# Kernel optimization log

Measured on AMD Instinct MI355X. Metric: run time of the kernel, lower is better.

The kernel has to match this reference:

```python
import jax, jax.numpy as jnp
import numpy as np

H = 16       # num heads
HD = 64      # head dim
D = H * HD   # hidden size

def _rotate_half(x):
    x1, x2 = jnp.split(x, 2, axis=-1)
    return jnp.concatenate([-x2, x1], axis=-1)

def setup_inputs() -> dict:
    key = jax.random.key(0)
    ks = jax.random.split(key, 12)
    B, N, NP = 16, 1029, 1024  # batch, tokens (5 prefix + 1024 patches), patch tokens
    inp = {
        "hidden_states": jax.random.normal(ks[0], (B, N, D), dtype=jnp.float32),
        "sin": jax.random.uniform(ks[1], (NP, HD), dtype=jnp.float32, minval=-1.0, maxval=1.0),
        "cos": jax.random.uniform(ks[2], (NP, HD), dtype=jnp.float32, minval=-1.0, maxval=1.0),
        "Wq": jax.random.normal(ks[3], (D, D), dtype=jnp.float32) * 0.02,
        "bq": jnp.zeros((D,), dtype=jnp.float32),
        "Wk": jax.random.normal(ks[4], (D, D), dtype=jnp.float32) * 0.02,
        "bk": jnp.zeros((D,), dtype=jnp.float32),
        "Wv": jax.random.normal(ks[5], (D, D), dtype=jnp.float32) * 0.02,
        "bv": jnp.zeros((D,), dtype=jnp.float32),
        "Wo": jax.random.normal(ks[6], (D, D), dtype=jnp.float32) * 0.02,
        "bo": jnp.zeros((D,), dtype=jnp.float32),
    }
    return inp

def reference(hidden_states, sin, cos, Wq, bq, Wk, bk, Wv, bv, Wo, bo):
    B, N, _ = hidden_states.shape
    scaling = HD ** -0.5
    # qkv projections (nn.Linear: x @ W.T + b), split to heads: [B,H,N,HD]
    def proj(W, b):
        y = hidden_states @ W.T + b
        return y.reshape(B, N, H, HD).transpose(0, 2, 1, 3)
    q, k, v = proj(Wq, bq), proj(Wk, bk), proj(Wv, bv)
    # rotary pos emb on patch-token suffix only
    prefix = N - sin.shape[-2]
    def rope(x):
        xs = x[:, :, prefix:, :]
        xs = xs * cos + _rotate_half(xs) * sin
        return jnp.concatenate([x[:, :, :prefix, :], xs], axis=2)
    q, k = rope(q), rope(k)
    # eager attention: softmax in fp32
    attn = jnp.einsum("bhqd,bhkd->bhqk", q, k) * scaling
    attn = jax.nn.softmax(attn.astype(jnp.float32), axis=-1).astype(q.dtype)
    out = jnp.einsum("bhqk,bhkd->bhqd", attn, v)
    out = out.transpose(0, 2, 1, 3).reshape(B, N, D)
    return out @ Wo.T + bo
```

## Files before the change

### kernel.cpp

```cpp
#include <hip/hip_runtime.h>
#include <stdint.h>

#define H 16
#define HD 64
#define D 1024
#define NTOK 1029
#define BATCH 16
#define NPAD 1152
#define M_ROWS (BATCH*NTOK)
#define MPAD 16512
#define KB 1024
#define PREFIX 5

typedef unsigned short u16;
typedef __attribute__((ext_vector_type(8))) short short8;
typedef __attribute__((ext_vector_type(4))) short short4v;
typedef __attribute__((ext_vector_type(4))) float float4v;
typedef __attribute__((ext_vector_type(4))) unsigned int uint4v;

__device__ __forceinline__ u16 f2bf(float x) {
  unsigned int u = __float_as_uint(x);
  u += 0x7FFFu + ((u >> 16) & 1u);
  return (u16)(u >> 16);
}

__device__ __forceinline__ void gload16(const void* g, void* l) {
  __builtin_amdgcn_global_load_lds((const __attribute__((address_space(1))) void*)g,
                                   (__attribute__((address_space(3))) void*)l, 16, 0, 0);
}

__global__ __launch_bounds__(256) void cvt_A_kernel(const float* __restrict__ src,
                                                    u16* __restrict__ dst) {
  int idx = blockIdx.x * 256 + threadIdx.x;
  int m = idx >> 8, k = (idx & 255) * 4;
  float4v x = (float4v)0.f;
  if (m < M_ROWS) x = *(const float4v*)(src + (size_t)m * D + k);
  short4v o;
#pragma unroll
  for (int j = 0; j < 4; j++) o[j] = (short)f2bf(x[j]);
  *(short4v*)(dst + (size_t)m * D + k) = o;
}

__global__ __launch_bounds__(256) void cvt_W_kernel(
    const float* __restrict__ w0, const float* __restrict__ w1,
    const float* __restrict__ w2, const float* __restrict__ w3,
    u16* __restrict__ e0, u16* __restrict__ e1, u16* __restrict__ e2, u16* __restrict__ e3) {
  const float* src = (blockIdx.y == 0) ? w0 : (blockIdx.y == 1) ? w1 : (blockIdx.y == 2) ? w2 : w3;
  u16* dst = (blockIdx.y == 0) ? e0 : (blockIdx.y == 1) ? e1 : (blockIdx.y == 2) ? e2 : e3;
  int idx = blockIdx.x * 256 + threadIdx.x;
  int m = idx >> 8, k = (idx & 255) * 4;
  float4v x = *(const float4v*)(src + (size_t)m * D + k);
  short4v o;
#pragma unroll
  for (int j = 0; j < 4; j++) o[j] = (short)f2bf(x[j]);
  *(short4v*)(dst + (size_t)m * D + k) = o;
}

__device__ __forceinline__ void gemm_mainloop(const u16* __restrict__ A,
                                              const u16* __restrict__ Bw,
                                              u16* As, u16* Bs, int mtile, int ntile,
                                              float4v acc[4][4]) {
  const int tid = threadIdx.x;
  const int lane = tid & 63;
  const int wave = tid >> 6;
  const int wm = (wave >> 1) * 64;
  const int wn = (wave & 1) * 64;
  const int ar = lane & 15;
  const int kq = lane >> 4;
#pragma unroll
  for (int i = 0; i < 4; i++)
#pragma unroll
    for (int j = 0; j < 4; j++) acc[i][j] = (float4v)0.f;

  const size_t abase = (size_t)mtile * 128 * KB;
  const size_t bbase = (size_t)ntile * 128 * KB;
  for (int k0 = 0; k0 < KB; k0 += 32) {
    __syncthreads();
#pragma unroll
    for (int i = 0; i < 2; i++) {
      int chunk = i * 256 + tid;
      gload16(A + abase + (size_t)(chunk >> 2) * KB + k0 + (chunk & 3) * 8,
              As + (size_t)(i * 256 + (tid & ~63)) * 8);
      gload16(Bw + bbase + (size_t)(chunk >> 2) * KB + k0 + (chunk & 3) * 8,
              Bs + (size_t)(i * 256 + (tid & ~63)) * 8);
    }
    __syncthreads();
    short8 af[4], bf[4];
#pragma unroll
    for (int ms = 0; ms < 4; ms++)
      af[ms] = *(const short8*)(As + (wm + ms * 16 + ar) * 32 + kq * 8);
#pragma unroll
    for (int ns = 0; ns < 4; ns++)
      bf[ns] = *(const short8*)(Bs + (wn + ns * 16 + ar) * 32 + kq * 8);
#pragma unroll
    for (int ms = 0; ms < 4; ms++)
#pragma unroll
      for (int ns = 0; ns < 4; ns++)
        acc[ms][ns] = __builtin_amdgcn_mfma_f32_16x16x32_bf16(af[ms], bf[ns], acc[ms][ns], 0, 0, 0);
  }
}

__global__ __launch_bounds__(256) void gemm_qkv_kernel(
    const u16* __restrict__ A,
    const u16* __restrict__ Wqb, const u16* __restrict__ Wkb, const u16* __restrict__ Wvb,
    const float* __restrict__ bq, const float* __restrict__ bk, const float* __restrict__ bv,
    const float* __restrict__ sinp, const float* __restrict__ cosp,
    u16* __restrict__ qb, u16* __restrict__ kb, u16* __restrict__ vt) {
  __shared__ __align__(16) u16 As[128 * 32];
  __shared__ __align__(16) u16 Bs[128 * 32];
  const int z = blockIdx.z;
  const u16* Bw = (z == 0) ? Wqb : (z == 1) ? Wkb : Wvb;
  const float* bias = (z == 0) ? bq : (z == 1) ? bk : bv;
  const int ntile = blockIdx.x, mtile = blockIdx.y;
  float4v acc[4][4];
  gemm_mainloop(A, Bw, As, Bs, mtile, ntile, acc);

  const int tid = threadIdx.x, lane = tid & 63, wave = tid >> 6;
  const int wm = (wave >> 1) * 64, wn = (wave & 1) * 64;
  const int ar = lane & 15, kq = lane >> 4;
#pragma unroll
  for (int ms = 0; ms < 4; ms++) {
#pragma unroll
    for (int r = 0; r < 4; r++) {
      int grow = mtile * 128 + wm + ms * 16 + kq * 4 + r;
      if (grow >= M_ROWS) continue;
      int b = grow / NTOK;
      int n = grow - b * NTOK;
      bool dorope = (z != 2) && (n >= PREFIX);
      int pos = n - PREFIX;
#pragma unroll
      for (int ns = 0; ns < 4; ns++) {
        int col = ntile * 128 + wn + ns * 16 + ar;
        int hh = col >> 6, d = col & 63;
        float y = acc[ms][ns][r] + bias[col];
        if (z == 2) {
          vt[((size_t)(b * H + hh) * 64 + d) * NPAD + n] = f2bf(y);
          continue;
        }
        if (dorope) {
          float xp = acc[ms][ns ^ 2][r] + bias[col ^ 32];
          float c = cosp[pos * HD + d], s = sinp[pos * HD + d];
          y = y * c + ((d < 32) ? -xp : xp) * s;
        }
        if (z == 0) y *= 0.125f;
        u16* outp = (z == 0) ? qb : kb;
        outp[((size_t)(b * H + hh) * NPAD + n) * 64 + d] = f2bf(y);
      }
    }
  }
}

#define SSHIFT 3.0f
#define NJT 17
__global__ __launch_bounds__(256) void attn_kernel(const u16* __restrict__ qb,
                                                   const u16* __restrict__ kb,
                                                   const u16* __restrict__ vt,
                                                   u16* __restrict__ ao) {
  __shared__ __align__(16) u16 sQ[128 * 72];
  __shared__ __align__(16) u16 sK[64 * 72];
  __shared__ __align__(16) u16 sV[64 * 72];
  const int tid = threadIdx.x, lane = tid & 63, wave = tid >> 6;
  const int ar = lane & 15, kq = lane >> 4;
  const int qt = blockIdx.x, hh = blockIdx.y, b = blockIdx.z;
  const int bh = b * H + hh;
  const u16* qbase = qb + (size_t)bh * NPAD * 64;
  const u16* kbase = kb + (size_t)bh * NPAD * 64;
  const u16* vbase = vt + (size_t)bh * 64 * NPAD;

#pragma unroll
  for (int i = 0; i < 4; i++) {
    int chunk = i * 256 + tid;
    int row = chunk >> 3, c = chunk & 7;
    *(uint4v*)(sQ + row * 72 + c * 8) =
        *(const uint4v*)(qbase + (size_t)(qt * 128 + row) * 64 + c * 8);
  }
  __syncthreads();
  short8 aq[2][2];
#pragma unroll
  for (int ms = 0; ms < 2; ms++)
#pragma unroll
    for (int ki = 0; ki < 2; ki++)
      aq[ms][ki] = *(const short8*)(sQ + (wave * 32 + ms * 16 + ar) * 72 + ki * 32 + kq * 8);
  u16* sP = sQ + wave * 32 * 72;

  float rs[2][4];
  float4v o_acc[2][4];
#pragma unroll
  for (int ms = 0; ms < 2; ms++)
#pragma unroll
    for (int r = 0; r < 4; r++) rs[ms][r] = 0.f;
#pragma unroll
  for (int ms = 0; ms < 2; ms++)
#pragma unroll
    for (int t = 0; t < 4; t++) o_acc[ms][t] = (float4v)0.f;

  for (int jt = 0; jt < NJT; jt++) {
    __syncthreads();
#pragma unroll
    for (int i = 0; i < 2; i++) {
      int chunk = i * 256 + tid;
      int row = chunk >> 3, c = chunk & 7;
      *(uint4v*)(sK + row * 72 + c * 8) =
          *(const uint4v*)(kbase + (size_t)(jt * 64 + row) * 64 + c * 8);
      *(uint4v*)(sV + row * 72 + c * 8) =
          *(const uint4v*)(vbase + (size_t)row * NPAD + jt * 64 + c * 8);
    }
    __syncthreads();

    float4v s[2][4];
#pragma unroll
    for (int ms = 0; ms < 2; ms++)
#pragma unroll
      for (int t = 0; t < 4; t++) s[ms][t] = (float4v)0.f;
#pragma unroll
    for (int ki = 0; ki < 2; ki++) {
#pragma unroll
      for (int t = 0; t < 4; t++) {
        short8 bk8 = *(const short8*)(sK + (t * 16 + ar) * 72 + ki * 32 + kq * 8);
#pragma unroll
        for (int ms = 0; ms < 2; ms++)
          s[ms][t] = __builtin_amdgcn_mfma_f32_16x16x32_bf16(aq[ms][ki], bk8, s[ms][t], 0, 0, 0);
      }
    }
    if (jt == NJT - 1) {
#pragma unroll
      for (int t = 0; t < 4; t++)
        if ((NJT - 1) * 64 + t * 16 + ar >= NTOK) {
#pragma unroll
          for (int ms = 0; ms < 2; ms++) s[ms][t] = (float4v)(-INFINITY);
        }
    }
    asm volatile("" ::: "memory");
#pragma unroll
    for (int ms = 0; ms < 2; ms++)
#pragma unroll
      for (int t = 0; t < 4; t++)
#pragma unroll
        for (int r = 0; r < 4; r++) {
          float p = __expf(s[ms][t][r] - SSHIFT);
          rs[ms][r] += p;
          sP[(ms * 16 + kq * 4 + r) * 72 + t * 16 + ar] = f2bf(p);
        }
    asm volatile("" ::: "memory");
#pragma unroll
    for (int ki = 0; ki < 2; ki++) {
#pragma unroll
      for (int ms = 0; ms < 2; ms++) {
        short8 ap = *(const short8*)(sP + (ms * 16 + ar) * 72 + ki * 32 + kq * 8);
#pragma unroll
        for (int t = 0; t < 4; t++) {
          short8 bv8 = *(const short8*)(sV + (t * 16 + ar) * 72 + ki * 32 + kq * 8);
          o_acc[ms][t] = __builtin_amdgcn_mfma_f32_16x16x32_bf16(ap, bv8, o_acc[ms][t], 0, 0, 0);
        }
      }
    }
  }
#pragma unroll
  for (int ms = 0; ms < 2; ms++)
#pragma unroll
    for (int r = 0; r < 4; r++) {
      float l = rs[ms][r];
#pragma unroll
      for (int off = 1; off < 16; off <<= 1) l += __shfl_xor(l, off, 64);
      int i = qt * 128 + wave * 32 + ms * 16 + kq * 4 + r;
      if (i >= NTOK) continue;
      float inv = 1.f / l;
      size_t mg = (size_t)b * NTOK + i;
#pragma unroll
      for (int t = 0; t < 4; t++)
        ao[mg * D + hh * 64 + t * 16 + ar] = f2bf(o_acc[ms][t][r] * inv);
    }
}

__global__ __launch_bounds__(256) void gemm_o_kernel(const u16* __restrict__ A,
                                                     const u16* __restrict__ Wob,
                                                     const float* __restrict__ bo,
                                                     float* __restrict__ out) {
  __shared__ __align__(16) u16 As[128 * 32];
  __shared__ __align__(16) u16 Bs[128 * 32];
  const int ntile = blockIdx.x, mtile = blockIdx.y;
  float4v acc[4][4];
  gemm_mainloop(A, Wob, As, Bs, mtile, ntile, acc);
  const int tid = threadIdx.x, lane = tid & 63, wave = tid >> 6;
  const int wm = (wave >> 1) * 64, wn = (wave & 1) * 64;
  const int ar = lane & 15, kq = lane >> 4;
#pragma unroll
  for (int ms = 0; ms < 4; ms++)
#pragma unroll
    for (int r = 0; r < 4; r++) {
      int grow = mtile * 128 + wm + ms * 16 + kq * 4 + r;
      if (grow >= M_ROWS) continue;
#pragma unroll
      for (int ns = 0; ns < 4; ns++) {
        int col = ntile * 128 + wn + ns * 16 + ar;
        out[(size_t)grow * D + col] = acc[ms][ns][r] + bo[col];
      }
    }
}

extern "C" void kernel_launch(void* const* d_in, const int* in_sizes, int n_in,
                              void* d_out, int out_size, void* d_ws, size_t ws_size,
                              hipStream_t stream) {
  const float* hidden = (const float*)d_in[0];
  const float* sinp = (const float*)d_in[1];
  const float* cosp = (const float*)d_in[2];
  const float* Wq = (const float*)d_in[3]; const float* bq = (const float*)d_in[4];
  const float* Wk = (const float*)d_in[5]; const float* bk = (const float*)d_in[6];
  const float* Wv = (const float*)d_in[7]; const float* bv = (const float*)d_in[8];
  const float* Wo = (const float*)d_in[9]; const float* bo = (const float*)d_in[10];
  float* out = (float*)d_out;
  (void)in_sizes; (void)n_in; (void)out_size; (void)ws_size;

  char* ws = (char*)d_ws;
  size_t off = 0;
  auto carve = [&](size_t elems) {
    u16* p = (u16*)(ws + off);
    off += ((elems * 2 + 255) & ~(size_t)255);
    return p;
  };
  u16* A_bf = carve((size_t)MPAD * KB);
  u16* Wqb = carve((size_t)D * KB);
  u16* Wkb = carve((size_t)D * KB);
  u16* Wvb = carve((size_t)D * KB);
  u16* Wob = carve((size_t)D * KB);
  u16* q_b = carve((size_t)BATCH * H * NPAD * 64);
  u16* k_b = carve((size_t)BATCH * H * NPAD * 64);
  u16* v_t = carve((size_t)BATCH * H * NPAD * 64);

  hipLaunchKernelGGL(cvt_A_kernel, dim3(MPAD), dim3(256), 0, stream, hidden, A_bf);
  hipLaunchKernelGGL(cvt_W_kernel, dim3(1024, 4), dim3(256), 0, stream,
                     Wq, Wk, Wv, Wo, Wqb, Wkb, Wvb, Wob);
  hipLaunchKernelGGL(gemm_qkv_kernel, dim3(8, 129, 3), dim3(256), 0, stream,
                     A_bf, Wqb, Wkb, Wvb, bq, bk, bv, sinp, cosp, q_b, k_b, v_t);
  hipLaunchKernelGGL(attn_kernel, dim3(9, H, BATCH), dim3(256), 0, stream, q_b, k_b, v_t, A_bf);
  hipLaunchKernelGGL(gemm_o_kernel, dim3(8, 129), dim3(256), 0, stream, A_bf, Wob, bo, out);
}
```

Before: 611.6 us.

## Rewrite projection GEMMs with 256x256 tiles, double-buffered LDS and swizzle

Replaces the 128x128, K=32 single-buffered GEMM mainloop with a 256x256 tile, K=64 stage, 8-wave kernel. Global-to-LDS loads are double-buffered and prefetched two stages ahead, and a XOR swizzle on the LDS layout avoids bank conflicts. Phased MFMA blocks use barriers and setprio to interleave the waves. This raises arithmetic intensity and overlaps loads with compute in both the QKV and output projections. It also uses much more LDS (128KB per block) and more registers, and pads MPAD so the 256-row tiles fit.

```diff
diff --git a/kernel.cpp b/kernel.cpp
--- a/kernel.cpp
+++ b/kernel.cpp
@@ -8,7 +8,8 @@
 #define BATCH 16
 #define NPAD 1152
 #define M_ROWS (BATCH*NTOK)
-#define MPAD 16512
+#define MPAD 16640
+#define MT256 65
 #define KB 1024
 #define PREFIX 5
 
@@ -56,73 +57,111 @@
   *(short4v*)(dst + (size_t)m * D + k) = o;
 }
 
-__device__ __forceinline__ void gemm_mainloop(const u16* __restrict__ A,
-                                              const u16* __restrict__ Bw,
-                                              u16* As, u16* Bs, int mtile, int ntile,
-                                              float4v acc[4][4]) {
+
+__device__ __forceinline__ void stage256(const u16* __restrict__ gA, const u16* __restrict__ gB,
+                                         u16* dA, u16* dB, int dwo) {
+#pragma unroll
+  for (int i = 0; i < 4; i++)
+    gload16(gA + (size_t)i * 64 * KB, dA + i * 4096 + dwo);
+#pragma unroll
+  for (int i = 0; i < 4; i++)
+    gload16(gB + (size_t)i * 64 * KB, dB + i * 4096 + dwo);
+}
+
+#define GPHASE(mh, soffv, loadB)                                                          \
+  {                                                                                       \
+    short8 afr[4];                                                                        \
+    _Pragma("unroll") for (int m4 = 0; m4 < 4; m4++)                                      \
+        afr[m4] = *(const short8*)(pA + (wm_idx * 128 + ((mh)*4 + m4) * 16 + ar) * 64 + (soffv)); \
+    if (loadB) {                                                                          \
+      _Pragma("unroll") for (int ns = 0; ns < 4; ns++)                                    \
+          bfr[ns] = *(const short8*)(pB + (wn_idx * 64 + ns * 16 + ar) * 64 + (soffv));   \
+    }                                                                                     \
+    __builtin_amdgcn_s_barrier();                                                         \
+    asm volatile("s_waitcnt lgkmcnt(0)" ::: "memory");                                    \
+    __builtin_amdgcn_s_setprio(1);                                                        \
+    _Pragma("unroll") for (int m4 = 0; m4 < 4; m4++) {                                    \
+      _Pragma("unroll") for (int ns = 0; ns < 4; ns++)                                    \
+        acc[(mh)*4 + m4][ns] = __builtin_amdgcn_mfma_f32_16x16x32_bf16(                   \
+            afr[m4], bfr[ns], acc[(mh)*4 + m4][ns], 0, 0, 0);                             \
+    }                                                                                     \
+    __builtin_amdgcn_s_setprio(0);                                                        \
+    __builtin_amdgcn_s_barrier();                                                         \
+  }
+
+__device__ __forceinline__ void gemm256_mainloop(const u16* __restrict__ A,
+                                                 const u16* __restrict__ Bw,
+                                                 u16 As[2][16384], u16 Bs[2][16384],
+                                                 int mtile, int ntile, float4v acc[8][4]) {
   const int tid = threadIdx.x;
   const int lane = tid & 63;
   const int wave = tid >> 6;
-  const int wm = (wave >> 1) * 64;
-  const int wn = (wave & 1) * 64;
+  const int wm_idx = wave >> 2;
+  const int wn_idx = wave & 3;
   const int ar = lane & 15;
   const int kq = lane >> 4;
-#pragma unroll
-  for (int i = 0; i < 4; i++)
+  const int s0 = ((kq)     ^ (ar & 7)) * 8;
+  const int s1 = ((4 + kq) ^ (ar & 7)) * 8;
+  const int srow = tid >> 3;
+  const int scol = ((tid & 7) ^ (srow & 7)) * 8;
+  const int dwo = (tid & ~63) * 8;
+  const size_t abase = (size_t)mtile * 256 * KB + (size_t)srow * KB + scol;
+  const size_t bbase = (size_t)ntile * 256 * KB + (size_t)srow * KB + scol;
+
+#pragma unroll
+  for (int i = 0; i < 8; i++)
 #pragma unroll
     for (int j = 0; j < 4; j++) acc[i][j] = (float4v)0.f;
 
-  const size_t abase = (size_t)mtile * 128 * KB;
-  const size_t bbase = (size_t)ntile * 128 * KB;
-  for (int k0 = 0; k0 < KB; k0 += 32) {
-    __syncthreads();
-#pragma unroll
-    for (int i = 0; i < 2; i++) {
-      int chunk = i * 256 + tid;
-      gload16(A + abase + (size_t)(chunk >> 2) * KB + k0 + (chunk & 3) * 8,
-              As + (size_t)(i * 256 + (tid & ~63)) * 8);
-      gload16(Bw + bbase + (size_t)(chunk >> 2) * KB + k0 + (chunk & 3) * 8,
-              Bs + (size_t)(i * 256 + (tid & ~63)) * 8);
-    }
-    __syncthreads();
-    short8 af[4], bf[4];
-#pragma unroll
-    for (int ms = 0; ms < 4; ms++)
-      af[ms] = *(const short8*)(As + (wm + ms * 16 + ar) * 32 + kq * 8);
-#pragma unroll
-    for (int ns = 0; ns < 4; ns++)
-      bf[ns] = *(const short8*)(Bs + (wn + ns * 16 + ar) * 32 + kq * 8);
-#pragma unroll
-    for (int ms = 0; ms < 4; ms++)
-#pragma unroll
-      for (int ns = 0; ns < 4; ns++)
-        acc[ms][ns] = __builtin_amdgcn_mfma_f32_16x16x32_bf16(af[ms], bf[ns], acc[ms][ns], 0, 0, 0);
-  }
-}
-
-__global__ __launch_bounds__(256) void gemm_qkv_kernel(
+  stage256(A + abase, Bw + bbase, As[0], Bs[0], dwo);
+  stage256(A + abase + 64, Bw + bbase + 64, As[1], Bs[1], dwo);
+  asm volatile("s_waitcnt vmcnt(8)" ::: "memory");
+  __builtin_amdgcn_s_barrier();
+
+  short8 bfr[4];
+  for (int t = 0; t < 16; ++t) {
+    const u16* pA = As[t & 1];
+    const u16* pB = Bs[t & 1];
+    GPHASE(0, s0, 1)
+    GPHASE(1, s0, 0)
+    GPHASE(0, s1, 1)
+    GPHASE(1, s1, 0)
+    if (t < 14) {
+      const int k0 = (t + 2) * 64;
+      stage256(A + abase + k0, Bw + bbase + k0, As[t & 1], Bs[t & 1], dwo);
+      asm volatile("s_waitcnt vmcnt(8)" ::: "memory");
+    } else {
+      asm volatile("s_waitcnt vmcnt(0)" ::: "memory");
+    }
+    __builtin_amdgcn_s_barrier();
+  }
+}
+
+__global__ __launch_bounds__(512, 2) void gemm_qkv_kernel(
     const u16* __restrict__ A,
     const u16* __restrict__ Wqb, const u16* __restrict__ Wkb, const u16* __restrict__ Wvb,
     const float* __restrict__ bq, const float* __restrict__ bk, const float* __restrict__ bv,
     const float* __restrict__ sinp, const float* __restrict__ cosp,
     u16* __restrict__ qb, u16* __restrict__ kb, u16* __restrict__ vt) {
-  __shared__ __align__(16) u16 As[128 * 32];
-  __shared__ __align__(16) u16 Bs[128 * 32];
+  __shared__ __align__(16) u16 As[2][16384];
+  __shared__ __align__(16) u16 Bs[2][16384];
   const int z = blockIdx.z;
   const u16* Bw = (z == 0) ? Wqb : (z == 1) ? Wkb : Wvb;
   const float* bias = (z == 0) ? bq : (z == 1) ? bk : bv;
   const int ntile = blockIdx.x, mtile = blockIdx.y;
-  float4v acc[4][4];
-  gemm_mainloop(A, Bw, As, Bs, mtile, ntile, acc);
+  float4v acc[8][4];
+  gemm256_mainloop(A, Bw, As, Bs, mtile, ntile, acc);
 
   const int tid = threadIdx.x, lane = tid & 63, wave = tid >> 6;
-  const int wm = (wave >> 1) * 64, wn = (wave & 1) * 64;
+  const int wm_idx = wave >> 2, wn_idx = wave & 3;
   const int ar = lane & 15, kq = lane >> 4;
-#pragma unroll
-  for (int ms = 0; ms < 4; ms++) {
+  const int rowb = mtile * 256 + wm_idx * 128;
+  const int colb = ntile * 256 + wn_idx * 64;
+#pragma unroll
+  for (int ms = 0; ms < 8; ms++) {
 #pragma unroll
     for (int r = 0; r < 4; r++) {
-      int grow = mtile * 128 + wm + ms * 16 + kq * 4 + r;
+      int grow = rowb + ms * 16 + kq * 4 + r;
       if (grow >= M_ROWS) continue;
       int b = grow / NTOK;
       int n = grow - b * NTOK;
@@ -130,7 +169,7 @@
       int pos = n - PREFIX;
 #pragma unroll
       for (int ns = 0; ns < 4; ns++) {
-        int col = ntile * 128 + wn + ns * 16 + ar;
+        int col = colb + ns * 16 + ar;
         int hh = col >> 6, d = col & 63;
         float y = acc[ms][ns][r] + bias[col];
         if (z == 2) {
@@ -272,30 +311,33 @@
     }
 }
 
-__global__ __launch_bounds__(256) void gemm_o_kernel(const u16* __restrict__ A,
-                                                     const u16* __restrict__ Wob,
-                                                     const float* __restrict__ bo,
-                                                     float* __restrict__ out) {
-  __shared__ __align__(16) u16 As[128 * 32];
-  __shared__ __align__(16) u16 Bs[128 * 32];
+__global__ __launch_bounds__(512, 2) void gemm_o_kernel(const u16* __restrict__ A,
+                                                        const u16* __restrict__ Wob,
+                                                        const float* __restrict__ bo,
+                                                        float* __restrict__ out) {
+  __shared__ __align__(16) u16 As[2][16384];
+  __shared__ __align__(16) u16 Bs[2][16384];
   const int ntile = blockIdx.x, mtile = blockIdx.y;
-  float4v acc[4][4];
-  gemm_mainloop(A, Wob, As, Bs, mtile, ntile, acc);
+  float4v acc[8][4];
+  gemm256_mainloop(A, Wob, As, Bs, mtile, ntile, acc);
   const int tid = threadIdx.x, lane = tid & 63, wave = tid >> 6;
-  const int wm = (wave >> 1) * 64, wn = (wave & 1) * 64;
+  const int wm_idx = wave >> 2, wn_idx = wave & 3;
   const int ar = lane & 15, kq = lane >> 4;
-#pragma unroll
-  for (int ms = 0; ms < 4; ms++)
+  const int rowb = mtile * 256 + wm_idx * 128;
+  const int colb = ntile * 256 + wn_idx * 64;
+#pragma unroll
+  for (int ms = 0; ms < 8; ms++) {
 #pragma unroll
     for (int r = 0; r < 4; r++) {
-      int grow = mtile * 128 + wm + ms * 16 + kq * 4 + r;
+      int grow = rowb + ms * 16 + kq * 4 + r;
       if (grow >= M_ROWS) continue;
 #pragma unroll
       for (int ns = 0; ns < 4; ns++) {
-        int col = ntile * 128 + wn + ns * 16 + ar;
+        int col = colb + ns * 16 + ar;
         out[(size_t)grow * D + col] = acc[ms][ns][r] + bo[col];
       }
     }
+  }
 }
 
 extern "C" void kernel_launch(void* const* d_in, const int* in_sizes, int n_in,
@@ -330,8 +372,8 @@
   hipLaunchKernelGGL(cvt_A_kernel, dim3(MPAD), dim3(256), 0, stream, hidden, A_bf);
   hipLaunchKernelGGL(cvt_W_kernel, dim3(1024, 4), dim3(256), 0, stream,
                      Wq, Wk, Wv, Wo, Wqb, Wkb, Wvb, Wob);
-  hipLaunchKernelGGL(gemm_qkv_kernel, dim3(8, 129, 3), dim3(256), 0, stream,
+  hipLaunchKernelGGL(gemm_qkv_kernel, dim3(4, MT256, 3), dim3(512), 0, stream,
                      A_bf, Wqb, Wkb, Wvb, bq, bk, bv, sinp, cosp, q_b, k_b, v_t);
   hipLaunchKernelGGL(attn_kernel, dim3(9, H, BATCH), dim3(256), 0, stream, q_b, k_b, v_t, A_bf);
-  hipLaunchKernelGGL(gemm_o_kernel, dim3(8, 129), dim3(256), 0, stream, A_bf, Wob, bo, out);
-}
+  hipLaunchKernelGGL(gemm_o_kernel, dim3(4, MT256), dim3(512), 0, stream, A_bf, Wob, bo, out);
+}
```

Result: slower. 694.8 us (+13.6%).
